# Kernel optimization log

Measured on AMD Instinct MI355X. Metric: run time of the kernel, lower is better.

Reference implementation:

```python
import jax, jax.numpy as jnp
import numpy as np

NUM_CLASSES = 20
NUM_ANCHORS = 5
INPUT_SIZE = 320.0
CONF_THR = 0.5
IOU_THR = 0.5
EPS = 1e-6
H = W = 40


def setup_inputs() -> dict:
    key = jax.random.key(0)
    x = jax.random.normal(key, (1, NUM_ANCHORS * (5 + NUM_CLASSES), H, W), dtype=jnp.float32)
    scaled_anchors = jnp.array(
        [[1.3221, 1.73145], [3.19275, 4.00944], [5.05587, 8.09892],
         [9.47112, 4.84053], [11.2364, 10.0071]], dtype=jnp.float32)
    return {"x": x, "scaled_anchors": scaled_anchors}


def decode(x, anchors):
    # x: (B, A*(5+C), H, W) -> boxes (B, A*H*W, 6) = [cx, cy, w, h, conf, cls]
    B, _, h, w = x.shape
    A = anchors.shape[0]
    stride_h = INPUT_SIZE / h
    stride_w = INPUT_SIZE / w
    pred = x.reshape(B, A, 5 + NUM_CLASSES, h, w).transpose(0, 1, 3, 4, 2)  # (B,A,H,W,5+C)
    tx = jax.nn.sigmoid(pred[..., 0])
    ty = jax.nn.sigmoid(pred[..., 1])
    tw = pred[..., 2]
    th = pred[..., 3]
    conf = jax.nn.sigmoid(pred[..., 4])
    cls_idx = jnp.argmax(jax.nn.sigmoid(pred[..., 5:]), axis=-1)  # (B,A,H,W)
    grid_x = jnp.arange(w, dtype=x.dtype)            # broadcasts along last axis
    grid_y = jnp.arange(h, dtype=x.dtype)[:, None]   # broadcasts along row axis
    aw = anchors[:, 0][None, :, None, None]
    ah = anchors[:, 1][None, :, None, None]
    bx = (tx + grid_x) * stride_w
    by = (ty + grid_y) * stride_h
    bw = jnp.exp(tw) * aw * stride_w
    bh = jnp.exp(th) * ah * stride_h
    boxes = jnp.stack([bx, by, bw, bh, conf], axis=-1).reshape(B, -1, 5)
    cls_f = cls_idx.reshape(B, -1, 1).astype(x.dtype)
    return jnp.concatenate([boxes, cls_f], axis=-1)


def nms(boxes6):
    # boxes6: (N, 6) [cx, cy, w, h, conf, cls]. Fixed-shape NMS: boxes are
    # sorted by conf desc; suppressed / low-conf boxes are zeroed out.
    order = jnp.argsort(-boxes6[:, 4])
    b = boxes6[order]
    valid = b[:, 4] > CONF_THR
    cx, cy, w, h, cls = b[:, 0], b[:, 1], b[:, 2], b[:, 3], b[:, 5]
    x1, y1 = cx - w / 2.0, cy - h / 2.0
    x2, y2 = cx + w / 2.0, cy + h / 2.0
    inter_w = jnp.clip(jnp.minimum(x2[:, None], x2[None, :]) - jnp.maximum(x1[:, None], x1[None, :]), 0)
    inter_h = jnp.clip(jnp.minimum(y2[:, None], y2[None, :]) - jnp.maximum(y1[:, None], y1[None, :]), 0)
    inter = inter_w * inter_h                       # (N, N)
    area = jnp.abs((x2 - x1) * (y2 - y1))
    iou = inter / (area[:, None] + area[None, :] - inter + EPS)
    N = b.shape[0]
    idx = jnp.arange(N)

    def body(i, keep):
        # kept box i suppresses later boxes of the same class with IoU >= thr
        sup = keep[i] & keep & (cls == cls[i]) & (iou[i] >= IOU_THR) & (idx > i)
        return keep & ~sup

    keep = jax.lax.fori_loop(0, N, body, valid)
    return b * keep[:, None].astype(b.dtype)


def reference(x, scaled_anchors):
    dec = decode(x, scaled_anchors)   # (1, N, 6)
    return nms(dec[0])                # (N, 6)
```

## Files before the change

kernel.cpp:

```cpp
#include <hip/hip_runtime.h>
#include <stdint.h>

#define NBOX 8000
#define NPAD 8192

#define ECNT_OFF 0
#define ALIVE_OFF 0x1000
#define SB(i)    (0x10000 + (size_t)(i) * 0x8000)
#define EDGE_OFF (size_t)0x200000

__device__ __forceinline__ float sigmoidf_(float x) {
    return 1.0f / (1.0f + expf(-x));
}

__global__ __launch_bounds__(512) void sort_decode_kernel(const float* __restrict__ x,
                                                          const float* __restrict__ anchors,
                                                          unsigned char* __restrict__ ws) {
    __shared__ unsigned long long keys[NPAD];
    __shared__ int partial[256];
    int tid  = threadIdx.x;
    int lane = tid & 63;
    int wv   = tid >> 6;
    int b    = blockIdx.x;

    if (b == 0 && tid == 0) *(unsigned int*)(ws + ECNT_OFF) = 0u;

    for (int t = tid; t < NPAD; t += 512) {
        unsigned long long k;
        if (t < NBOX) {
            int a = t / 1600, pos = t - a * 1600;
            float c = sigmoidf_(x[a * 40000 + 4 * 1600 + pos]);
            k = ((unsigned long long)__float_as_uint(c) << 32) | (unsigned long long)(8191 - t);
        } else {
            k = (unsigned long long)(8191 - t);
        }
        keys[t] = k;
    }
    __syncthreads();

    unsigned long long kj[16];
    #pragma unroll
    for (int c = 0; c < 16; ++c) kj[c] = keys[(wv << 10) + (c << 6) + lane];
    unsigned long long ki = keys[(b << 5) + lane];

    int vout = 0;
    for (int ii = 0; ii < 32; ++ii) {
        unsigned int klo = (unsigned int)__builtin_amdgcn_readlane((int)(unsigned int)ki, ii);
        unsigned int khi = (unsigned int)__builtin_amdgcn_readlane((int)(unsigned int)(ki >> 32), ii);
        unsigned long long kib = ((unsigned long long)khi << 32) | (unsigned long long)klo;
        int c = 0;
        #pragma unroll
        for (int ch = 0; ch < 16; ++ch)
            c += __popcll(__ballot(kj[ch] > kib));
        vout = (lane == ii) ? c : vout;
    }
    if (lane < 32) partial[(wv << 5) + lane] = vout;
    __syncthreads();

    if (wv == 0 && lane < 32) {
        int r = 0;
        #pragma unroll
        for (int s = 0; s < 8; ++s) r += partial[(s << 5) + lane];

        int i = (b << 5) + lane;
        float bx = 0.f, by = 0.f, bw = 0.f, bh = 0.f, conf = 0.f, cls = -1.0f;
        if (i < NBOX) {
            int a = i / 1600, pos = i - a * 1600;
            int gy = pos / 40, gx = pos - gy * 40;
            const float* p = x + (size_t)a * 40000 + pos;
            float tx = sigmoidf_(p[0]);
            float ty = sigmoidf_(p[1600]);
            float tw = p[2 * 1600];
            float th = p[3 * 1600];
            conf = sigmoidf_(p[4 * 1600]);
            float best = -1.0f; int bi = 0;
            #pragma unroll
            for (int c = 0; c < 20; ++c) {
                float v = sigmoidf_(p[(5 + c) * 1600]);
                if (v > best) { best = v; bi = c; }
            }
            float aw = anchors[a * 2 + 0];
            float ah = anchors[a * 2 + 1];
            bx = (tx + (float)gx) * 8.0f;
            by = (ty + (float)gy) * 8.0f;
            bw = expf(tw) * aw * 8.0f;
            bh = expf(th) * ah * 8.0f;
            cls = (float)bi;
        }
        {
        #pragma clang fp contract(off)
            float x1 = bx - bw / 2.0f, y1 = by - bh / 2.0f;
            float x2 = bx + bw / 2.0f, y2 = by + bh / 2.0f;
            float ar = fabsf((x2 - x1) * (y2 - y1));
            ((float*)(ws + SB(0)))[r]  = bx;  ((float*)(ws + SB(1)))[r]  = by;
            ((float*)(ws + SB(2)))[r]  = bw;  ((float*)(ws + SB(3)))[r]  = bh;
            ((float*)(ws + SB(4)))[r]  = conf; ((float*)(ws + SB(5)))[r] = cls;
            ((float*)(ws + SB(6)))[r]  = x1;  ((float*)(ws + SB(7)))[r]  = y1;
            ((float*)(ws + SB(8)))[r]  = x2;  ((float*)(ws + SB(9)))[r]  = y2;
            ((float*)(ws + SB(10)))[r] = ar;
        }
    }
}

__global__ __launch_bounds__(256) void mask_kernel(unsigned char* __restrict__ ws) {
#pragma clang fp contract(off)
    const float* sconf = (const float*)(ws + SB(4));
    int i0 = blockIdx.y * 256;
    int w  = blockIdx.x;
    int j0 = w * 64;
    if (sconf[i0] <= 0.5f) return;
    if (sconf[j0] <= 0.5f) return;
    if (j0 + 64 <= i0) return;
    int tid  = threadIdx.x;
    int lane = tid & 63;
    int i    = i0 + tid;

    const float* sx1 = (const float*)(ws + SB(6));
    const float* sy1 = (const float*)(ws + SB(7));
    const float* sx2 = (const float*)(ws + SB(8));
    const float* sy2 = (const float*)(ws + SB(9));
    const float* sar = (const float*)(ws + SB(10));
    const float* scl = (const float*)(ws + SB(5));

    __shared__ float cx1[64], cy1[64], cx2[64], cy2[64], car[64], ccl[64], ccf[64];
    if (tid < 64) {
        int j = j0 + tid;
        cx1[tid] = sx1[j]; cy1[tid] = sy1[j];
        cx2[tid] = sx2[j]; cy2[tid] = sy2[j];
        car[tid] = sar[j]; ccl[tid] = scl[j]; ccf[tid] = sconf[j];
    }
    __syncthreads();

    unsigned long long word = 0;
    if (sconf[i] > 0.5f && j0 + 64 > i + 1) {
        float x1i = sx1[i], y1i = sy1[i], x2i = sx2[i], y2i = sy2[i];
        float ai = sar[i], ci = scl[i];
        for (int jj = 0; jj < 64; ++jj) {
            int j = j0 + jj;
            if (j <= i) continue;
            if (ccf[jj] <= 0.5f) continue;
            if (ccl[jj] != ci) continue;
            float iw = fminf(x2i, cx2[jj]) - fmaxf(x1i, cx1[jj]);
            iw = fmaxf(iw, 0.0f);
            float ih = fminf(y2i, cy2[jj]) - fmaxf(y1i, cy1[jj]);
            ih = fmaxf(ih, 0.0f);
            float inter = iw * ih;
            float denom = ai + car[jj] - inter + 1e-6f;
            if (inter / denom >= 0.5f) word |= (1ull << jj);
        }
    }

    int pc = __popcll(word);
    int scan = pc;
    #pragma unroll
    for (int d = 1; d < 64; d <<= 1) {
        int t = __shfl_up(scan, d, 64);
        if (lane >= d) scan += t;
    }
    int total = __shfl(scan, 63, 64);
    if (total > 0) {
        unsigned int base = 0;
        if (lane == 63)
            base = atomicAdd((unsigned int*)(ws + ECNT_OFF), (unsigned int)total);
        base = (unsigned int)__shfl((int)base, 63, 64);
        unsigned int off = base + (unsigned int)(scan - pc);
        unsigned int* edges = (unsigned int*)(ws + EDGE_OFF);
        unsigned long long t = word;
        while (t) {
            int bit = __builtin_ctzll(t);
            t &= t - 1ull;
            edges[off++] = ((unsigned int)i << 13) | (unsigned int)(j0 + bit);
        }
    }
}

#define ELDS 32768
__global__ __launch_bounds__(1024, 1) void nms_kernel(unsigned char* __restrict__ ws) {
    int tid  = threadIdx.x;
    int lane = tid & 63;
    unsigned int E = *(const unsigned int*)(ws + ECNT_OFF);
    const unsigned int* edges = (const unsigned int*)(ws + EDGE_OFF);
    const float* sconf = (const float*)(ws + SB(4));

    __shared__ unsigned long long valid[128], alive[128], supp[128];
    __shared__ int flag;
    __shared__ unsigned int eld[ELDS];

    for (int c = tid >> 6; c < 128; c += 16) {
        unsigned long long m = __ballot(sconf[(c << 6) + lane] > 0.5f);
        if (lane == 0) valid[c] = m;
    }
    bool uselds = (E <= (unsigned int)ELDS);
    if (uselds)
        for (unsigned int e = tid; e < E; e += 1024) eld[e] = edges[e];
    __syncthreads();
    if (tid < 128) alive[tid] = valid[tid];
    __syncthreads();

    for (;;) {
        if (tid < 128) supp[tid] = 0ull;
        __syncthreads();
        if (uselds) {
            for (unsigned int e = tid; e < E; e += 1024) {
                unsigned int u = eld[e];
                unsigned int i = u >> 13, j = u & 8191u;
                if ((alive[i >> 6] >> (i & 63)) & 1ull)
                    atomicOr(&supp[j >> 6], 1ull << (j & 63));
            }
        } else {
            for (unsigned int e = tid; e < E; e += 1024) {
                unsigned int u = edges[e];
                unsigned int i = u >> 13, j = u & 8191u;
                if ((alive[i >> 6] >> (i & 63)) & 1ull)
                    atomicOr(&supp[j >> 6], 1ull << (j & 63));
            }
        }
        if (tid == 0) flag = 0;
        __syncthreads();
        if (tid < 128) {
            unsigned long long na = valid[tid] & ~supp[tid];
            if (na != alive[tid]) { alive[tid] = na; flag = 1; }
        }
        __syncthreads();
        if (!flag) break;
    }

    if (tid < 128) ((unsigned long long*)(ws + ALIVE_OFF))[tid] = alive[tid];
}

__global__ __launch_bounds__(256) void out_kernel(const unsigned char* __restrict__ ws,
                                                  float* __restrict__ out) {
    __shared__ float o[256 * 6];
    int tid = threadIdx.x;
    int r0  = blockIdx.x << 8;
    int r   = r0 + tid;
    const unsigned long long* alive = (const unsigned long long*)(ws + ALIVE_OFF);

    float v0 = 0.f, v1 = 0.f, v2 = 0.f, v3 = 0.f, v4 = 0.f, v5 = 0.f;
    if (r < NBOX && ((alive[r >> 6] >> (r & 63)) & 1ull)) {
        v0 = ((const float*)(ws + SB(0)))[r];
        v1 = ((const float*)(ws + SB(1)))[r];
        v2 = ((const float*)(ws + SB(2)))[r];
        v3 = ((const float*)(ws + SB(3)))[r];
        v4 = ((const float*)(ws + SB(4)))[r];
        v5 = ((const float*)(ws + SB(5)))[r];
    }
    o[tid * 6 + 0] = v0; o[tid * 6 + 1] = v1; o[tid * 6 + 2] = v2;
    o[tid * 6 + 3] = v3; o[tid * 6 + 4] = v4; o[tid * 6 + 5] = v5;
    __syncthreads();

    int base = r0 * 6;
    for (int t = tid; t < 256 * 6; t += 256) {
        int idx = base + t;
        if (idx < NBOX * 6) out[idx] = o[t];
    }
}

extern "C" void kernel_launch(void* const* d_in, const int* in_sizes, int n_in,
                              void* d_out, int out_size, void* d_ws, size_t ws_size,
                              hipStream_t stream) {
    const float* x       = (const float*)d_in[0];
    const float* anchors = (const float*)d_in[1];
    float* out           = (float*)d_out;
    unsigned char* ws    = (unsigned char*)d_ws;

    sort_decode_kernel<<<NPAD / 32, 512, 0, stream>>>(x, anchors, ws);
    dim3 mgrid(128, NPAD / 256);
    mask_kernel<<<mgrid, 256, 0, stream>>>(ws);
    nms_kernel<<<1, 1024, 0, stream>>>(ws);
    out_kernel<<<32, 256, 0, stream>>>(ws, out);
}
```

Baseline: 111.0 us.

## Fuse decode, mask, NMS and output kernels into one cooperative kernel

Merges the four separate kernels into a single cooperative launch of 256 blocks, using grid-wide syncs between the sort/decode, IoU mask, iterative NMS and output phases. Shared memory is unioned across phases and the mask work is redistributed so each block handles 8 tiles in two halves. The goal is to remove three kernel launch gaps. In exchange it adds grid.sync barriers, and the single-block NMS phase now runs with 512 threads and a smaller LDS edge cache (16384 entries), so it falls back to global memory more often.

After: 275.1 us. +147.9%, slower.

```diff
diff --git a/kernel.cpp b/kernel.cpp
--- a/kernel.cpp
+++ b/kernel.cpp
@@ -1,5 +1,8 @@
 #include <hip/hip_runtime.h>
+#include <hip/hip_cooperative_groups.h>
 #include <stdint.h>
+
+namespace cg = cooperative_groups;
 
 #define NBOX 8000
 #define NPAD 8192
@@ -13,246 +16,244 @@
     return 1.0f / (1.0f + expf(-x));
 }
 
-__global__ __launch_bounds__(512) void sort_decode_kernel(const float* __restrict__ x,
-                                                          const float* __restrict__ anchors,
-                                                          unsigned char* __restrict__ ws) {
-    __shared__ unsigned long long keys[NPAD];
-    __shared__ int partial[256];
+__global__ __launch_bounds__(512, 1) void yolo_nms_fused(const float* __restrict__ x,
+                                                         const float* __restrict__ anchors,
+                                                         unsigned char* __restrict__ ws,
+                                                         float* __restrict__ out) {
+    __shared__ union {
+        struct { unsigned long long keys[NPAD]; int partial[256]; } a;
+        struct { float cst[2][7][64]; } b;
+        struct { unsigned int eld[16384];
+                 unsigned long long valid[128], alive[128], supp[128];
+                 int flag; } c;
+        struct { float o[192]; } d;
+    } u;
+
+    cg::grid_group grid = cg::this_grid();
     int tid  = threadIdx.x;
     int lane = tid & 63;
     int wv   = tid >> 6;
-    int b    = blockIdx.x;
-
-    if (b == 0 && tid == 0) *(unsigned int*)(ws + ECNT_OFF) = 0u;
-
-    for (int t = tid; t < NPAD; t += 512) {
-        unsigned long long k;
-        if (t < NBOX) {
-            int a = t / 1600, pos = t - a * 1600;
-            float c = sigmoidf_(x[a * 40000 + 4 * 1600 + pos]);
-            k = ((unsigned long long)__float_as_uint(c) << 32) | (unsigned long long)(8191 - t);
-        } else {
-            k = (unsigned long long)(8191 - t);
-        }
-        keys[t] = k;
-    }
-    __syncthreads();
-
-    unsigned long long kj[16];
-    #pragma unroll
-    for (int c = 0; c < 16; ++c) kj[c] = keys[(wv << 10) + (c << 6) + lane];
-    unsigned long long ki = keys[(b << 5) + lane];
-
-    int vout = 0;
-    for (int ii = 0; ii < 32; ++ii) {
-        unsigned int klo = (unsigned int)__builtin_amdgcn_readlane((int)(unsigned int)ki, ii);
-        unsigned int khi = (unsigned int)__builtin_amdgcn_readlane((int)(unsigned int)(ki >> 32), ii);
-        unsigned long long kib = ((unsigned long long)khi << 32) | (unsigned long long)klo;
-        int c = 0;
+    int blk  = blockIdx.x;
+
+    {
+        if (blk == 0 && tid == 0) *(unsigned int*)(ws + ECNT_OFF) = 0u;
+
+        for (int t = tid; t < NPAD; t += 512) {
+            unsigned long long k;
+            if (t < NBOX) {
+                int a = t / 1600, pos = t - a * 1600;
+                float c = sigmoidf_(x[a * 40000 + 4 * 1600 + pos]);
+                k = ((unsigned long long)__float_as_uint(c) << 32) | (unsigned long long)(8191 - t);
+            } else {
+                k = (unsigned long long)(8191 - t);
+            }
+            u.a.keys[t] = k;
+        }
+        __syncthreads();
+
+        unsigned long long kj[16];
         #pragma unroll
-        for (int ch = 0; ch < 16; ++ch)
-            c += __popcll(__ballot(kj[ch] > kib));
-        vout = (lane == ii) ? c : vout;
-    }
-    if (lane < 32) partial[(wv << 5) + lane] = vout;
-    __syncthreads();
-
-    if (wv == 0 && lane < 32) {
-        int r = 0;
-        #pragma unroll
-        for (int s = 0; s < 8; ++s) r += partial[(s << 5) + lane];
-
-        int i = (b << 5) + lane;
-        float bx = 0.f, by = 0.f, bw = 0.f, bh = 0.f, conf = 0.f, cls = -1.0f;
-        if (i < NBOX) {
-            int a = i / 1600, pos = i - a * 1600;
-            int gy = pos / 40, gx = pos - gy * 40;
-            const float* p = x + (size_t)a * 40000 + pos;
-            float tx = sigmoidf_(p[0]);
-            float ty = sigmoidf_(p[1600]);
-            float tw = p[2 * 1600];
-            float th = p[3 * 1600];
-            conf = sigmoidf_(p[4 * 1600]);
-            float best = -1.0f; int bi = 0;
+        for (int c = 0; c < 16; ++c) kj[c] = u.a.keys[(wv << 10) + (c << 6) + lane];
+        unsigned long long ki = u.a.keys[(blk << 5) + lane];
+
+        int vout = 0;
+        for (int ii = 0; ii < 32; ++ii) {
+            unsigned int klo = (unsigned int)__builtin_amdgcn_readlane((int)(unsigned int)ki, ii);
+            unsigned int khi = (unsigned int)__builtin_amdgcn_readlane((int)(unsigned int)(ki >> 32), ii);
+            unsigned long long kib = ((unsigned long long)khi << 32) | (unsigned long long)klo;
+            int c = 0;
             #pragma unroll
-            for (int c = 0; c < 20; ++c) {
-                float v = sigmoidf_(p[(5 + c) * 1600]);
-                if (v > best) { best = v; bi = c; }
-            }
-            float aw = anchors[a * 2 + 0];
-            float ah = anchors[a * 2 + 1];
-            bx = (tx + (float)gx) * 8.0f;
-            by = (ty + (float)gy) * 8.0f;
-            bw = expf(tw) * aw * 8.0f;
-            bh = expf(th) * ah * 8.0f;
-            cls = (float)bi;
-        }
-        {
-        #pragma clang fp contract(off)
-            float x1 = bx - bw / 2.0f, y1 = by - bh / 2.0f;
-            float x2 = bx + bw / 2.0f, y2 = by + bh / 2.0f;
-            float ar = fabsf((x2 - x1) * (y2 - y1));
-            ((float*)(ws + SB(0)))[r]  = bx;  ((float*)(ws + SB(1)))[r]  = by;
-            ((float*)(ws + SB(2)))[r]  = bw;  ((float*)(ws + SB(3)))[r]  = bh;
-            ((float*)(ws + SB(4)))[r]  = conf; ((float*)(ws + SB(5)))[r] = cls;
-            ((float*)(ws + SB(6)))[r]  = x1;  ((float*)(ws + SB(7)))[r]  = y1;
-            ((float*)(ws + SB(8)))[r]  = x2;  ((float*)(ws + SB(9)))[r]  = y2;
-            ((float*)(ws + SB(10)))[r] = ar;
-        }
-    }
-}
-
-__global__ __launch_bounds__(256) void mask_kernel(unsigned char* __restrict__ ws) {
-#pragma clang fp contract(off)
-    const float* sconf = (const float*)(ws + SB(4));
-    int i0 = blockIdx.y * 256;
-    int w  = blockIdx.x;
-    int j0 = w * 64;
-    if (sconf[i0] <= 0.5f) return;
-    if (sconf[j0] <= 0.5f) return;
-    if (j0 + 64 <= i0) return;
-    int tid  = threadIdx.x;
-    int lane = tid & 63;
-    int i    = i0 + tid;
-
-    const float* sx1 = (const float*)(ws + SB(6));
-    const float* sy1 = (const float*)(ws + SB(7));
-    const float* sx2 = (const float*)(ws + SB(8));
-    const float* sy2 = (const float*)(ws + SB(9));
-    const float* sar = (const float*)(ws + SB(10));
-    const float* scl = (const float*)(ws + SB(5));
-
-    __shared__ float cx1[64], cy1[64], cx2[64], cy2[64], car[64], ccl[64], ccf[64];
-    if (tid < 64) {
-        int j = j0 + tid;
-        cx1[tid] = sx1[j]; cy1[tid] = sy1[j];
-        cx2[tid] = sx2[j]; cy2[tid] = sy2[j];
-        car[tid] = sar[j]; ccl[tid] = scl[j]; ccf[tid] = sconf[j];
-    }
-    __syncthreads();
-
-    unsigned long long word = 0;
-    if (sconf[i] > 0.5f && j0 + 64 > i + 1) {
-        float x1i = sx1[i], y1i = sy1[i], x2i = sx2[i], y2i = sy2[i];
-        float ai = sar[i], ci = scl[i];
-        for (int jj = 0; jj < 64; ++jj) {
-            int j = j0 + jj;
-            if (j <= i) continue;
-            if (ccf[jj] <= 0.5f) continue;
-            if (ccl[jj] != ci) continue;
-            float iw = fminf(x2i, cx2[jj]) - fmaxf(x1i, cx1[jj]);
-            iw = fmaxf(iw, 0.0f);
-            float ih = fminf(y2i, cy2[jj]) - fmaxf(y1i, cy1[jj]);
-            ih = fmaxf(ih, 0.0f);
-            float inter = iw * ih;
-            float denom = ai + car[jj] - inter + 1e-6f;
-            if (inter / denom >= 0.5f) word |= (1ull << jj);
-        }
-    }
-
-    int pc = __popcll(word);
-    int scan = pc;
-    #pragma unroll
-    for (int d = 1; d < 64; d <<= 1) {
-        int t = __shfl_up(scan, d, 64);
-        if (lane >= d) scan += t;
-    }
-    int total = __shfl(scan, 63, 64);
-    if (total > 0) {
-        unsigned int base = 0;
-        if (lane == 63)
-            base = atomicAdd((unsigned int*)(ws + ECNT_OFF), (unsigned int)total);
-        base = (unsigned int)__shfl((int)base, 63, 64);
-        unsigned int off = base + (unsigned int)(scan - pc);
-        unsigned int* edges = (unsigned int*)(ws + EDGE_OFF);
-        unsigned long long t = word;
-        while (t) {
-            int bit = __builtin_ctzll(t);
-            t &= t - 1ull;
-            edges[off++] = ((unsigned int)i << 13) | (unsigned int)(j0 + bit);
-        }
-    }
-}
-
-#define ELDS 32768
-__global__ __launch_bounds__(1024, 1) void nms_kernel(unsigned char* __restrict__ ws) {
-    int tid  = threadIdx.x;
-    int lane = tid & 63;
-    unsigned int E = *(const unsigned int*)(ws + ECNT_OFF);
-    const unsigned int* edges = (const unsigned int*)(ws + EDGE_OFF);
-    const float* sconf = (const float*)(ws + SB(4));
-
-    __shared__ unsigned long long valid[128], alive[128], supp[128];
-    __shared__ int flag;
-    __shared__ unsigned int eld[ELDS];
-
-    for (int c = tid >> 6; c < 128; c += 16) {
-        unsigned long long m = __ballot(sconf[(c << 6) + lane] > 0.5f);
-        if (lane == 0) valid[c] = m;
-    }
-    bool uselds = (E <= (unsigned int)ELDS);
-    if (uselds)
-        for (unsigned int e = tid; e < E; e += 1024) eld[e] = edges[e];
-    __syncthreads();
-    if (tid < 128) alive[tid] = valid[tid];
-    __syncthreads();
-
-    for (;;) {
-        if (tid < 128) supp[tid] = 0ull;
-        __syncthreads();
-        if (uselds) {
-            for (unsigned int e = tid; e < E; e += 1024) {
-                unsigned int u = eld[e];
-                unsigned int i = u >> 13, j = u & 8191u;
-                if ((alive[i >> 6] >> (i & 63)) & 1ull)
-                    atomicOr(&supp[j >> 6], 1ull << (j & 63));
-            }
-        } else {
-            for (unsigned int e = tid; e < E; e += 1024) {
-                unsigned int u = edges[e];
-                unsigned int i = u >> 13, j = u & 8191u;
-                if ((alive[i >> 6] >> (i & 63)) & 1ull)
-                    atomicOr(&supp[j >> 6], 1ull << (j & 63));
-            }
-        }
-        if (tid == 0) flag = 0;
-        __syncthreads();
-        if (tid < 128) {
-            unsigned long long na = valid[tid] & ~supp[tid];
-            if (na != alive[tid]) { alive[tid] = na; flag = 1; }
-        }
-        __syncthreads();
-        if (!flag) break;
-    }
-
-    if (tid < 128) ((unsigned long long*)(ws + ALIVE_OFF))[tid] = alive[tid];
-}
-
-__global__ __launch_bounds__(256) void out_kernel(const unsigned char* __restrict__ ws,
-                                                  float* __restrict__ out) {
-    __shared__ float o[256 * 6];
-    int tid = threadIdx.x;
-    int r0  = blockIdx.x << 8;
-    int r   = r0 + tid;
-    const unsigned long long* alive = (const unsigned long long*)(ws + ALIVE_OFF);
-
-    float v0 = 0.f, v1 = 0.f, v2 = 0.f, v3 = 0.f, v4 = 0.f, v5 = 0.f;
-    if (r < NBOX && ((alive[r >> 6] >> (r & 63)) & 1ull)) {
-        v0 = ((const float*)(ws + SB(0)))[r];
-        v1 = ((const float*)(ws + SB(1)))[r];
-        v2 = ((const float*)(ws + SB(2)))[r];
-        v3 = ((const float*)(ws + SB(3)))[r];
-        v4 = ((const float*)(ws + SB(4)))[r];
-        v5 = ((const float*)(ws + SB(5)))[r];
-    }
-    o[tid * 6 + 0] = v0; o[tid * 6 + 1] = v1; o[tid * 6 + 2] = v2;
-    o[tid * 6 + 3] = v3; o[tid * 6 + 4] = v4; o[tid * 6 + 5] = v5;
-    __syncthreads();
-
-    int base = r0 * 6;
-    for (int t = tid; t < 256 * 6; t += 256) {
-        int idx = base + t;
-        if (idx < NBOX * 6) out[idx] = o[t];
+            for (int ch = 0; ch < 16; ++ch)
+                c += __popcll(__ballot(kj[ch] > kib));
+            vout = (lane == ii) ? c : vout;
+        }
+        if (lane < 32) u.a.partial[(wv << 5) + lane] = vout;
+        __syncthreads();
+
+        if (wv == 0 && lane < 32) {
+            int r = 0;
+            #pragma unroll
+            for (int s = 0; s < 8; ++s) r += u.a.partial[(s << 5) + lane];
+
+            int i = (blk << 5) + lane;
+            float bx = 0.f, by = 0.f, bw = 0.f, bh = 0.f, conf = 0.f, cls = -1.0f;
+            if (i < NBOX) {
+                int a = i / 1600, pos = i - a * 1600;
+                int gy = pos / 40, gx = pos - gy * 40;
+                const float* p = x + (size_t)a * 40000 + pos;
+                float tx = sigmoidf_(p[0]);
+                float ty = sigmoidf_(p[1600]);
+                float tw = p[2 * 1600];
+                float th = p[3 * 1600];
+                conf = sigmoidf_(p[4 * 1600]);
+                float best = -1.0f; int bi = 0;
+                #pragma unroll
+                for (int c = 0; c < 20; ++c) {
+                    float v = sigmoidf_(p[(5 + c) * 1600]);
+                    if (v > best) { best = v; bi = c; }
+                }
+                float aw = anchors[a * 2 + 0];
+                float ah = anchors[a * 2 + 1];
+                bx = (tx + (float)gx) * 8.0f;
+                by = (ty + (float)gy) * 8.0f;
+                bw = expf(tw) * aw * 8.0f;
+                bh = expf(th) * ah * 8.0f;
+                cls = (float)bi;
+            }
+            {
+            #pragma clang fp contract(off)
+                float x1 = bx - bw / 2.0f, y1 = by - bh / 2.0f;
+                float x2 = bx + bw / 2.0f, y2 = by + bh / 2.0f;
+                float ar = fabsf((x2 - x1) * (y2 - y1));
+                ((float*)(ws + SB(0)))[r]  = bx;  ((float*)(ws + SB(1)))[r]  = by;
+                ((float*)(ws + SB(2)))[r]  = bw;  ((float*)(ws + SB(3)))[r]  = bh;
+                ((float*)(ws + SB(4)))[r]  = conf; ((float*)(ws + SB(5)))[r] = cls;
+                ((float*)(ws + SB(6)))[r]  = x1;  ((float*)(ws + SB(7)))[r]  = y1;
+                ((float*)(ws + SB(8)))[r]  = x2;  ((float*)(ws + SB(9)))[r]  = y2;
+                ((float*)(ws + SB(10)))[r] = ar;
+            }
+        }
+    }
+    __threadfence();
+    grid.sync();
+
+    {
+    #pragma clang fp contract(off)
+        const float* sconf = (const float*)(ws + SB(4));
+        const float* sx1 = (const float*)(ws + SB(6));
+        const float* sy1 = (const float*)(ws + SB(7));
+        const float* sx2 = (const float*)(ws + SB(8));
+        const float* sy2 = (const float*)(ws + SB(9));
+        const float* sar = (const float*)(ws + SB(10));
+        const float* scl = (const float*)(ws + SB(5));
+
+        int h  = tid >> 8;
+        int tl = tid & 255;
+
+        for (int k = 0; k < 8; ++k) {
+            int t  = k * 512 + (blk << 1) + h;
+            int iy = t >> 7, w = t & 127;
+            int i0 = iy << 8, j0 = w << 6;
+            bool skip = (sconf[i0] <= 0.5f) || (sconf[j0] <= 0.5f) || (j0 + 64 <= i0);
+
+            if (!skip && tl < 64) {
+                int j = j0 + tl;
+                u.b.cst[h][0][tl] = sx1[j]; u.b.cst[h][1][tl] = sy1[j];
+                u.b.cst[h][2][tl] = sx2[j]; u.b.cst[h][3][tl] = sy2[j];
+                u.b.cst[h][4][tl] = sar[j]; u.b.cst[h][5][tl] = scl[j];
+                u.b.cst[h][6][tl] = sconf[j];
+            }
+            __syncthreads();
+
+            if (!skip) {
+                int i = i0 + tl;
+                unsigned long long word = 0;
+                if (sconf[i] > 0.5f && j0 + 64 > i + 1) {
+                    float x1i = sx1[i], y1i = sy1[i], x2i = sx2[i], y2i = sy2[i];
+                    float ai = sar[i], ci = scl[i];
+                    for (int jj = 0; jj < 64; ++jj) {
+                        int j = j0 + jj;
+                        if (j <= i) continue;
+                        if (u.b.cst[h][6][jj] <= 0.5f) continue;
+                        if (u.b.cst[h][5][jj] != ci) continue;
+                        float iw = fminf(x2i, u.b.cst[h][2][jj]) - fmaxf(x1i, u.b.cst[h][0][jj]);
+                        iw = fmaxf(iw, 0.0f);
+                        float ih = fminf(y2i, u.b.cst[h][3][jj]) - fmaxf(y1i, u.b.cst[h][1][jj]);
+                        ih = fmaxf(ih, 0.0f);
+                        float inter = iw * ih;
+                        float denom = ai + u.b.cst[h][4][jj] - inter + 1e-6f;
+                        if (inter / denom >= 0.5f) word |= (1ull << jj);
+                    }
+                }
+                int pc = __popcll(word);
+                int scan = pc;
+                #pragma unroll
+                for (int d = 1; d < 64; d <<= 1) {
+                    int tt = __shfl_up(scan, d, 64);
+                    if (lane >= d) scan += tt;
+                }
+                int total = __shfl(scan, 63, 64);
+                if (total > 0) {
+                    unsigned int base = 0;
+                    if (lane == 63)
+                        base = atomicAdd((unsigned int*)(ws + ECNT_OFF), (unsigned int)total);
+                    base = (unsigned int)__shfl((int)base, 63, 64);
+                    unsigned int off = base + (unsigned int)(scan - pc);
+                    unsigned int* edges = (unsigned int*)(ws + EDGE_OFF);
+                    unsigned long long tw = word;
+                    while (tw) {
+                        int bit = __builtin_ctzll(tw);
+                        tw &= tw - 1ull;
+                        edges[off++] = ((unsigned int)i << 13) | (unsigned int)(j0 + bit);
+                    }
+                }
+            }
+            __syncthreads();
+        }
+    }
+    __threadfence();
+    grid.sync();
+
+    if (blk == 0) {
+        unsigned int E = *(const unsigned int*)(ws + ECNT_OFF);
+        const unsigned int* edges = (const unsigned int*)(ws + EDGE_OFF);
+        const float* sconf = (const float*)(ws + SB(4));
+
+        for (int c = tid >> 6; c < 128; c += 8) {
+            unsigned long long m = __ballot(sconf[(c << 6) + lane] > 0.5f);
+            if (lane == 0) u.c.valid[c] = m;
+        }
+        bool uselds = (E <= 16384u);
+        if (uselds)
+            for (unsigned int e = tid; e < E; e += 512) u.c.eld[e] = edges[e];
+        __syncthreads();
+        if (tid < 128) u.c.alive[tid] = u.c.valid[tid];
+        __syncthreads();
+
+        for (;;) {
+            if (tid < 128) u.c.supp[tid] = 0ull;
+            __syncthreads();
+            for (unsigned int e = tid; e < E; e += 512) {
+                unsigned int uu = uselds ? u.c.eld[e] : edges[e];
+                unsigned int i = uu >> 13, j = uu & 8191u;
+                if ((u.c.alive[i >> 6] >> (i & 63)) & 1ull)
+                    atomicOr(&u.c.supp[j >> 6], 1ull << (j & 63));
+            }
+            if (tid == 0) u.c.flag = 0;
+            __syncthreads();
+            if (tid < 128) {
+                unsigned long long na = u.c.valid[tid] & ~u.c.supp[tid];
+                if (na != u.c.alive[tid]) { u.c.alive[tid] = na; u.c.flag = 1; }
+            }
+            __syncthreads();
+            if (!u.c.flag) break;
+        }
+
+        if (tid < 128) ((unsigned long long*)(ws + ALIVE_OFF))[tid] = u.c.alive[tid];
+        __threadfence();
+    }
+    grid.sync();
+
+    {
+        const unsigned long long* alv = (const unsigned long long*)(ws + ALIVE_OFF);
+        int r0 = blk << 5;
+        if (tid < 32) {
+            int r = r0 + tid;
+            float v0 = 0.f, v1 = 0.f, v2 = 0.f, v3 = 0.f, v4 = 0.f, v5 = 0.f;
+            if ((alv[r >> 6] >> (r & 63)) & 1ull) {
+                v0 = ((const float*)(ws + SB(0)))[r];
+                v1 = ((const float*)(ws + SB(1)))[r];
+                v2 = ((const float*)(ws + SB(2)))[r];
+                v3 = ((const float*)(ws + SB(3)))[r];
+                v4 = ((const float*)(ws + SB(4)))[r];
+                v5 = ((const float*)(ws + SB(5)))[r];
+            }
+            u.d.o[tid * 6 + 0] = v0; u.d.o[tid * 6 + 1] = v1; u.d.o[tid * 6 + 2] = v2;
+            u.d.o[tid * 6 + 3] = v3; u.d.o[tid * 6 + 4] = v4; u.d.o[tid * 6 + 5] = v5;
+        }
+        __syncthreads();
+        int base = r0 * 6;
+        if (tid < 192 && base + tid < NBOX * 6) out[base + tid] = u.d.o[tid];
     }
 }
 
@@ -264,9 +265,7 @@
     float* out           = (float*)d_out;
     unsigned char* ws    = (unsigned char*)d_ws;
 
-    sort_decode_kernel<<<NPAD / 32, 512, 0, stream>>>(x, anchors, ws);
-    dim3 mgrid(128, NPAD / 256);
-    mask_kernel<<<mgrid, 256, 0, stream>>>(ws);
-    nms_kernel<<<1, 1024, 0, stream>>>(ws);
-    out_kernel<<<32, 256, 0, stream>>>(ws, out);
+    void* args[] = { (void*)&x, (void*)&anchors, (void*)&ws, (void*)&out };
+    hipLaunchCooperativeKernel((const void*)yolo_nms_fused, dim3(256), dim3(512),
+                               args, 0, stream);
 }
```
